# Kernel optimization log

Hardware: AMD Instinct MI355X
Metric: run time of the kernel (lower is better)

The kernel has to match this reference:

```python
import jax, jax.numpy as jnp
import numpy as np

H = 16          # n_heads
EPS = 1e-3      # keras LayerNormalization default epsilon


def _layernorm(x, gamma, beta):
    m = jnp.mean(x, axis=-1, keepdims=True)
    v = jnp.var(x, axis=-1, keepdims=True)
    return (x - m) * jax.lax.rsqrt(v + EPS) * gamma + beta


def _mha(q, k, v, wq, bq, wk, bk, wv, bv, wo, bo, causal):
    B, Sq, D = q.shape
    Sk = k.shape[1]
    d = D // H
    qh = (q @ wq + bq).reshape(B, Sq, H, d)
    kh = (k @ wk + bk).reshape(B, Sk, H, d)
    vh = (v @ wv + bv).reshape(B, Sk, H, d)
    scores = jnp.einsum('bqhd,bkhd->bhqk', qh, kh) / jnp.sqrt(jnp.asarray(d, qh.dtype))
    if causal:
        mask = jnp.tril(jnp.ones((Sq, Sk), dtype=bool))
        scores = jnp.where(mask, scores, jnp.asarray(-1e9, scores.dtype))
    attn = jax.nn.softmax(scores, axis=-1)
    out = jnp.einsum('bhqk,bkhd->bqhd', attn, vh).reshape(B, Sq, D)
    return out @ wo + bo


def setup_inputs() -> dict:
    key = jax.random.key(0)
    B, S, D, DFF = 4, 1024, 1024, 4096
    ks = jax.random.split(key, 16)
    sc = 0.02
    inp = {
        'inputs': jax.random.normal(ks[0], (B, S, D), jnp.float32),
        'enc_outputs': jax.random.normal(ks[1], (B, S, D), jnp.float32),
    }
    # self-attention (mha1)
    inp['wq1'] = jax.random.normal(ks[2], (D, D), jnp.float32) * sc
    inp['wk1'] = jax.random.normal(ks[3], (D, D), jnp.float32) * sc
    inp['wv1'] = jax.random.normal(ks[4], (D, D), jnp.float32) * sc
    inp['wo1'] = jax.random.normal(ks[5], (D, D), jnp.float32) * sc
    inp['bq1'] = jnp.zeros((D,), jnp.float32)
    inp['bk1'] = jnp.zeros((D,), jnp.float32)
    inp['bv1'] = jnp.zeros((D,), jnp.float32)
    inp['bo1'] = jnp.zeros((D,), jnp.float32)
    # cross-attention (mha2)
    inp['wq2'] = jax.random.normal(ks[6], (D, D), jnp.float32) * sc
    inp['wk2'] = jax.random.normal(ks[7], (D, D), jnp.float32) * sc
    inp['wv2'] = jax.random.normal(ks[8], (D, D), jnp.float32) * sc
    inp['wo2'] = jax.random.normal(ks[9], (D, D), jnp.float32) * sc
    inp['bq2'] = jnp.zeros((D,), jnp.float32)
    inp['bk2'] = jnp.zeros((D,), jnp.float32)
    inp['bv2'] = jnp.zeros((D,), jnp.float32)
    inp['bo2'] = jnp.zeros((D,), jnp.float32)
    # FFN
    inp['w_ff1'] = jax.random.normal(ks[10], (D, DFF), jnp.float32) * sc
    inp['b_ff1'] = jnp.zeros((DFF,), jnp.float32)
    inp['w_ff2'] = jax.random.normal(ks[11], (DFF, D), jnp.float32) * sc
    inp['b_ff2'] = jnp.zeros((D,), jnp.float32)
    # LayerNorms
    for i in (1, 2, 3):
        inp[f'g{i}'] = jnp.ones((D,), jnp.float32)
        inp[f'be{i}'] = jnp.zeros((D,), jnp.float32)
    return inp


def reference(inputs, enc_outputs,
              wq1, bq1, wk1, bk1, wv1, bv1, wo1, bo1,
              wq2, bq2, wk2, bk2, wv2, bv2, wo2, bo2,
              w_ff1, b_ff1, w_ff2, b_ff2,
              g1, be1, g2, be2, g3, be3):
    # self-attention block (causal) + residual + LN; dropout is identity (eval)
    a1 = _mha(inputs, inputs, inputs, wq1, bq1, wk1, bk1, wv1, bv1, wo1, bo1, causal=True)
    o1 = _layernorm(inputs + a1, g1, be1)
    # cross-attention block + residual + LN
    a2 = _mha(o1, enc_outputs, enc_outputs, wq2, bq2, wk2, bk2, wv2, bv2, wo2, bo2, causal=False)
    o2 = _layernorm(o1 + a2, g2, be2)
    # FFN block + residual + LN
    f = jax.nn.relu(o2 @ w_ff1 + b_ff1) @ w_ff2 + b_ff2
    return _layernorm(o2 + f, g3, be3)
```

## Files before the change

kernel.cpp:

```cpp
#include <hip/hip_runtime.h>
#include <stdint.h>
#include <stddef.h>

typedef __attribute__((ext_vector_type(4))) float  floatx4;
typedef __attribute__((ext_vector_type(8))) short  short8;
typedef __attribute__((ext_vector_type(4))) short  short4v;

__device__ __forceinline__ float bf2f(short s) {
  union { uint32_t u; float f; } v;
  v.u = ((uint32_t)(uint16_t)s) << 16;
  return v.f;
}
__device__ __forceinline__ short f2bf(float f) {
  union { float f; uint32_t u; } v; v.f = f;
  uint32_t r = v.u + 0x7fffu + ((v.u >> 16) & 1u);
  return (short)(r >> 16);
}

__device__ __forceinline__ void async_cp16(const void* g, void* l) {
  __builtin_amdgcn_global_load_lds(
      (__attribute__((address_space(1))) void*)g,
      (__attribute__((address_space(3))) void*)l, 16, 0, 0);
}

__device__ __forceinline__ int swzb(int row, int bcol) {
  return ((row << 7) + bcol) ^ ((row & 7) << 4);
}

struct TransTable {
  const float* src[10];
  short*       dst[10];
  int K[10], N[10], base[10];
};
__global__ __launch_bounds__(256)
void transpose_all(TransTable tt)
{
  __shared__ short tile[32][33];
  int e = 0;
  #pragma unroll
  for (int i = 1; i < 10; i++) if ((int)blockIdx.x >= tt.base[i]) e = i;
  const int t = blockIdx.x - tt.base[e];
  const int N = tt.N[e], K = tt.K[e];
  const int ncols = N >> 5;
  const int n0 = (t % ncols) << 5, k0 = (t / ncols) << 5;
  const float* src = tt.src[e];
  short* dst = tt.dst[e];
  const int tx = threadIdx.x & 31, ty = threadIdx.x >> 5;
  #pragma unroll
  for (int i = 0; i < 32; i += 8)
    tile[ty + i][tx] = f2bf(src[(size_t)(k0 + ty + i) * N + n0 + tx]);
  __syncthreads();
  #pragma unroll
  for (int i = 0; i < 32; i += 8)
    dst[(size_t)(n0 + ty + i) * K + k0 + tx] = tile[tx][ty + i];
}

__global__ __launch_bounds__(256)
void convert_xe(const float* __restrict__ x, const float* __restrict__ enc,
                short* __restrict__ xc, short* __restrict__ encc)
{
  int b = blockIdx.x;
  const float* s; short* d;
  if (b < 4096) { s = x; d = xc; } else { s = enc; d = encc; b -= 4096; }
  const int i = (b * 256 + threadIdx.x) * 4;
  const floatx4 v = *(const floatx4*)(s + i);
  short4v o;
  #pragma unroll
  for (int j = 0; j < 4; j++) o[j] = f2bf(v[j]);
  *(short4v*)(d + i) = o;
}

struct ParamMap { const float* s[19]; int off[19]; };
__global__ __launch_bounds__(256)
void convert_params(ParamMap pm, short* __restrict__ dst)
{
  const int b = blockIdx.x;
  for (int t = threadIdx.x; t < 1024; t += 256)
    dst[b * 1024 + t] = f2bf(pm.s[b][pm.off[b] + t]);
}

__device__ __forceinline__ void xcd2d(int nbn, int& bm, int& bn) {
  const int x   = (int)blockIdx.x & 7;
  const int loc = (int)blockIdx.x >> 3;
  const int nbm = ((int)gridDim.x) / nbn;
  const int gm  = nbm >> 2;
  const int gn  = nbn >> 1;
  bm = (x >> 1) * gm + loc / gn;
  bn = (x & 1) * gn + loc % gn;
}

template<int RELU, int RESID, int BM, int BN>
__global__ __launch_bounds__(256)
void gemm_bt(const short* __restrict__ A, const short* __restrict__ BT,
             const short* __restrict__ bias, const short* __restrict__ resid,
             short* __restrict__ C, int M, int N, int K)
{
  constexpr int MT = BM / 32;
  constexpr int NT = BN / 32;
  __shared__ short8 As0[BM * 4];
  __shared__ short8 As1[BM * 4];
  __shared__ short8 Bs0[BN * 4];
  __shared__ short8 Bs1[BN * 4];
  const int tid  = threadIdx.x;
  const int w    = tid >> 6;
  const int lane = tid & 63;
  const int m16  = lane & 15;
  const int g    = lane >> 4;
  const int nbn  = N / BN;
  int bm, bn;
  xcd2d(nbn, bm, bn);
  const int wm   = (w >> 1) * (BM / 2);
  const int wn   = (w & 1) * (BN / 2);

  const int r0 = lane >> 2;
  const int c0 = lane & 3;
  const int csw = c0 ^ ((r0 >> 1) & 3);
  const short* pA = A  + (size_t)(bm * BM + w * (BM / 4) + r0) * K + csw * 8;
  const short* pB = BT + (size_t)(bn * BN + w * (BN / 4) + r0) * K + csw * 8;

  floatx4 acc[MT][NT];
  #pragma unroll
  for (int i = 0; i < MT; i++)
    #pragma unroll
    for (int j = 0; j < NT; j++)
      acc[i][j] = floatx4{0.f, 0.f, 0.f, 0.f};

  auto stage = [&](short8* AS, short8* BS, int k0) {
    async_cp16(pA + k0, AS + w * BM);
    if constexpr (BM == 128) async_cp16(pA + k0 + 16 * (size_t)K, AS + w * BM + 64);
    async_cp16(pB + k0, BS + w * BN);
    if constexpr (BN == 128) async_cp16(pB + k0 + 16 * (size_t)K, BS + w * BN + 64);
  };
  const int gs = g ^ ((m16 >> 1) & 3);
  auto compute = [&](const short8* AS, const short8* BS) {
    short8 af[MT], bfr[NT];
    #pragma unroll
    for (int mt = 0; mt < MT; mt++)
      af[mt] = AS[(wm + mt * 16 + m16) * 4 + gs];
    #pragma unroll
    for (int nt = 0; nt < NT; nt++)
      bfr[nt] = BS[(wn + nt * 16 + m16) * 4 + gs];
    #pragma unroll
    for (int mt = 0; mt < MT; mt++)
      #pragma unroll
      for (int nt = 0; nt < NT; nt++)
        acc[mt][nt] = __builtin_amdgcn_mfma_f32_16x16x32_bf16(af[mt], bfr[nt], acc[mt][nt], 0, 0, 0);
  };

  stage(As0, Bs0, 0);
  __syncthreads();

  for (int k0 = 0; k0 < K; k0 += 64) {
    stage(As1, Bs1, k0 + 32);
    compute(As0, Bs0);
    __syncthreads();
    if (k0 + 64 < K)
      stage(As0, Bs0, k0 + 64);
    compute(As1, Bs1);
    __syncthreads();
  }

  #pragma unroll
  for (int mt = 0; mt < MT; mt++) {
    const int rbase = bm * BM + wm + mt * 16 + g * 4;
    #pragma unroll
    for (int nt = 0; nt < NT; nt++) {
      const int col = bn * BN + wn + nt * 16 + m16;
      const float bia = bf2f(bias[col]);
      #pragma unroll
      for (int r = 0; r < 4; r++) {
        const size_t idx = (size_t)(rbase + r) * N + col;
        float v = acc[mt][nt][r] + bia;
        if (RESID) v += bf2f(resid[idx]);
        if (RELU)  v = fmaxf(v, 0.f);
        C[idx] = f2bf(v);
      }
    }
  }
}

template<int RELU, int RESID>
__global__ __launch_bounds__(256)
void gemm_bt64(const short* __restrict__ A, const short* __restrict__ BT,
               const short* __restrict__ bias, const short* __restrict__ resid,
               short* __restrict__ C, int M, int N, int K)
{
  __shared__ short8 As0[512], As1[512];
  __shared__ short8 Bs0[512], Bs1[512];
  const int tid  = threadIdx.x;
  const int w    = tid >> 6;
  const int lane = tid & 63;
  const int m16  = lane & 15;
  const int g    = lane >> 4;
  const int nbn  = N >> 6;
  int bm, bn;
  xcd2d(nbn, bm, bn);
  const int wm   = (w >> 1) << 5;
  const int wn   = (w & 1) << 5;

  const int r0  = lane >> 3;
  const int c0  = lane & 7;
  const int csw = c0 ^ r0;
  const short* pA = A  + (size_t)(bm * 64 + w * 16 + r0) * K + csw * 8;
  const short* pB = BT + (size_t)(bn * 64 + w * 16 + r0) * K + csw * 8;

  floatx4 acc[2][2];
  #pragma unroll
  for (int i = 0; i < 2; i++)
    #pragma unroll
    for (int j = 0; j < 2; j++)
      acc[i][j] = floatx4{0.f, 0.f, 0.f, 0.f};

  auto stage = [&](short8* AS, short8* BS, int k0) {
    async_cp16(pA + k0,                 AS + w * 128);
    async_cp16(pA + k0 + 8 * (size_t)K, AS + w * 128 + 64);
    async_cp16(pB + k0,                 BS + w * 128);
    async_cp16(pB + k0 + 8 * (size_t)K, BS + w * 128 + 64);
  };
  const int sw = m16 & 7;
  auto compute = [&](const short8* AS, const short8* BS) {
    #pragma unroll
    for (int s = 0; s < 2; s++) {
      const int pc = (4 * s + g) ^ sw;
      short8 af[2], bfr[2];
      #pragma unroll
      for (int mt = 0; mt < 2; mt++)
        af[mt] = AS[(wm + mt * 16 + m16) * 8 + pc];
      #pragma unroll
      for (int nt = 0; nt < 2; nt++)
        bfr[nt] = BS[(wn + nt * 16 + m16) * 8 + pc];
      #pragma unroll
      for (int mt = 0; mt < 2; mt++)
        #pragma unroll
        for (int nt = 0; nt < 2; nt++)
          acc[mt][nt] = __builtin_amdgcn_mfma_f32_16x16x32_bf16(af[mt], bfr[nt], acc[mt][nt], 0, 0, 0);
    }
  };

  stage(As0, Bs0, 0);
  __syncthreads();

  for (int k0 = 0; k0 < K; k0 += 128) {
    stage(As1, Bs1, k0 + 64);
    compute(As0, Bs0);
    __syncthreads();
    if (k0 + 128 < K)
      stage(As0, Bs0, k0 + 128);
    compute(As1, Bs1);
    __syncthreads();
  }

  #pragma unroll
  for (int mt = 0; mt < 2; mt++) {
    const int rbase = bm * 64 + wm + mt * 16 + g * 4;
    #pragma unroll
    for (int nt = 0; nt < 2; nt++) {
      const int col = bn * 64 + wn + nt * 16 + m16;
      const float bia = bf2f(bias[col]);
      #pragma unroll
      for (int r = 0; r < 4; r++) {
        const size_t idx = (size_t)(rbase + r) * N + col;
        float v = acc[mt][nt][r] + bia;
        if (RESID) v += bf2f(resid[idx]);
        if (RELU)  v = fmaxf(v, 0.f);
        C[idx] = f2bf(v);
      }
    }
  }
}

template<int CAUSAL>
__global__ __launch_bounds__(256, 4)
void attention(const short* __restrict__ Qp, int ldq,
               const short* __restrict__ Kp, int ldk,
               const short* __restrict__ Vp, int ldv,
               short* __restrict__ Op, int ldo)
{
  const int S   = 1024;
  const int bid = (((int)blockIdx.x & 7) << 7) | ((int)blockIdx.x >> 3);
  const int qt  = bid & 15;
  const int h   = (bid >> 4) & 15;
  const int b   = bid >> 8;
  const int tid = threadIdx.x;
  const int w   = tid >> 6;
  const int lane = tid & 63;
  const int m16 = lane & 15;
  const int g   = lane >> 4;

  __shared__ __align__(16) short Ks[2][64 * 64];
  __shared__ __align__(16) short VT[2][64 * 64];
  __shared__ __align__(16) short Ps[4][16 * 64];

  const int rowQ = b * S + qt * 64;
  const int wrow = w * 16;

  const short* qsrc = Qp + (size_t)(rowQ + wrow + m16) * ldq + h * 64 + 8 * g;
  const short8 qf0 = *(const short8*)qsrc;
  const short8 qf1 = *(const short8*)(qsrc + 32);

  float mrow = -1e38f;
  float lrow = 0.f;
  floatx4 oacc[4];
  #pragma unroll
  for (int dt = 0; dt < 4; dt++) oacc[dt] = floatx4{0.f, 0.f, 0.f, 0.f};

  const int kr  = tid >> 2, kc = (tid & 3) << 4;
  const int vkp = (tid & 31) * 2, vcg = (tid >> 5) << 3;

  const short* kbase = Kp + (size_t)(b * S + kr)  * ldk + h * 64 + kc;
  const short* vbase = Vp + (size_t)(b * S + vkp) * ldv + h * 64 + vcg;

  const int nkt = CAUSAL ? (qt + 1) : (S / 64);
  const int qi  = qt * 64 + wrow + m16;

  short8 kst0 = *(const short8*)kbase;
  short8 kst1 = *(const short8*)(kbase + 8);
  short8 vst0 = *(const short8*)vbase;
  short8 vst1 = *(const short8*)(vbase + ldv);
  {
    char* kd = (char*)&Ks[0][0];
    *(short8*)(kd + swzb(kr, kc * 2))      = kst0;
    *(short8*)(kd + swzb(kr, kc * 2 + 16)) = kst1;
    char* vd = (char*)&VT[0][0];
    #pragma unroll
    for (int j = 0; j < 8; j++) {
      const uint32_t pk = (uint32_t)(uint16_t)vst0[j] | ((uint32_t)(uint16_t)vst1[j] << 16);
      *(uint32_t*)(vd + swzb(vcg + j, vkp * 2)) = pk;
    }
  }
  __syncthreads();

  for (int kt = 0; kt < nkt; kt++) {
    const int cur  = kt & 1;
    const int more = (kt + 1 < nkt);

    if (more) {
      const size_t roff = (size_t)(kt + 1) * 64;
      kst0 = *(const short8*)(kbase + roff * ldk);
      kst1 = *(const short8*)(kbase + roff * ldk + 8);
      vst0 = *(const short8*)(vbase + roff * ldv);
      vst1 = *(const short8*)(vbase + roff * ldv + ldv);
    }

    const int kb = kt * 64;

    const char* ksrc = (const char*)&Ks[cur][0];
    floatx4 sc[4];
    #pragma unroll
    for (int cg4 = 0; cg4 < 4; cg4++) {
      const short8 kfa = *(const short8*)(ksrc + swzb(cg4 * 16 + m16, 16 * g));
      const short8 kfb = *(const short8*)(ksrc + swzb(cg4 * 16 + m16, 64 + 16 * g));
      sc[cg4] = __builtin_amdgcn_mfma_f32_16x16x32_bf16(kfa, qf0, floatx4{0.f,0.f,0.f,0.f}, 0, 0, 0);
      sc[cg4] = __builtin_amdgcn_mfma_f32_16x16x32_bf16(kfb, qf1, sc[cg4], 0, 0, 0);
    }

    float v4[4][4];
    #pragma unroll
    for (int cg = 0; cg < 4; cg++)
      #pragma unroll
      for (int r = 0; r < 4; r++) {
        float x = sc[cg][r] * 0.125f;
        if (CAUSAL && kt == qt) {
          const int key = kb + cg * 16 + g * 4 + r;
          if (key > qi) x = -1e9f;
        }
        v4[cg][r] = x;
      }

    float mx = v4[0][0];
    #pragma unroll
    for (int cg = 0; cg < 4; cg++)
      #pragma unroll
      for (int r = 0; r < 4; r++) mx = fmaxf(mx, v4[cg][r]);
    mx = fmaxf(mx, __shfl_xor(mx, 16));
    mx = fmaxf(mx, __shfl_xor(mx, 32));
    const float mn = fmaxf(mrow, mx);
    const float alpha = __expf(mrow - mn);
    mrow = mn;

    float rs = 0.f;
    #pragma unroll
    for (int cg = 0; cg < 4; cg++)
      #pragma unroll
      for (int r = 0; r < 4; r++) { v4[cg][r] = __expf(v4[cg][r] - mn); rs += v4[cg][r]; }
    rs += __shfl_xor(rs, 16);
    rs += __shfl_xor(rs, 32);
    lrow = lrow * alpha + rs;

    #pragma unroll
    for (int r = 0; r < 4; r++) {
      const float aR = __shfl(alpha, (g << 2) | r);
      #pragma unroll
      for (int dt = 0; dt < 4; dt++) oacc[dt][r] *= aR;
    }

    char* pbase = (char*)&Ps[w][0];
    #pragma unroll
    for (int cg = 0; cg < 4; cg++) {
      const uint32_t p0 = (uint32_t)(uint16_t)f2bf(v4[cg][0]) |
                          ((uint32_t)(uint16_t)f2bf(v4[cg][1]) << 16);
      const uint32_t p1 = (uint32_t)(uint16_t)f2bf(v4[cg][2]) |
                          ((uint32_t)(uint16_t)f2bf(v4[cg][3]) << 16);
      *(uint32_t*)(pbase + swzb(m16, (8 * cg + 2 * g) * 4))     = p0;
      *(uint32_t*)(pbase + swzb(m16, (8 * cg + 2 * g + 1) * 4)) = p1;
    }

    asm volatile("s_waitcnt lgkmcnt(0)" ::: "memory");
    __builtin_amdgcn_sched_barrier(0);

    const short8 pf0 = *(const short8*)(pbase + swzb(m16, 16 * g));
    const short8 pf1 = *(const short8*)(pbase + swzb(m16, 64 + 16 * g));
    const char* vsrc = (const char*)&VT[cur][0];
    #pragma unroll
    for (int dt = 0; dt < 4; dt++) {
      const short8 vfa = *(const short8*)(vsrc + swzb(dt * 16 + m16, 16 * g));
      const short8 vfb = *(const short8*)(vsrc + swzb(dt * 16 + m16, 64 + 16 * g));
      oacc[dt] = __builtin_amdgcn_mfma_f32_16x16x32_bf16(pf0, vfa, oacc[dt], 0, 0, 0);
      oacc[dt] = __builtin_amdgcn_mfma_f32_16x16x32_bf16(pf1, vfb, oacc[dt], 0, 0, 0);
    }

    if (more) {
      char* kd = (char*)&Ks[cur ^ 1][0];
      *(short8*)(kd + swzb(kr, kc * 2))      = kst0;
      *(short8*)(kd + swzb(kr, kc * 2 + 16)) = kst1;
      char* vd = (char*)&VT[cur ^ 1][0];
      #pragma unroll
      for (int j = 0; j < 8; j++) {
        const uint32_t pk = (uint32_t)(uint16_t)vst0[j] | ((uint32_t)(uint16_t)vst1[j] << 16);
        *(uint32_t*)(vd + swzb(vcg + j, vkp * 2)) = pk;
      }
      __syncthreads();
    }
  }

  float lR[4];
  #pragma unroll
  for (int r = 0; r < 4; r++) lR[r] = __shfl(lrow, (g << 2) | r);
  #pragma unroll
  for (int dt = 0; dt < 4; dt++)
    #pragma unroll
    for (int r = 0; r < 4; r++) {
      const size_t orow = (size_t)(rowQ + wrow + g * 4 + r);
      Op[orow * ldo + h * 64 + dt * 16 + m16] = f2bf(oacc[dt][r] / lR[r]);
    }
}

template<int FINAL>
__global__ __launch_bounds__(256)
void layernorm_bf16(const short* __restrict__ x, const short* __restrict__ gamma,
                    const short* __restrict__ beta, void* __restrict__ out)
{
  const int D = 1024;
  const int row = blockIdx.x, tid = threadIdx.x;
  const short* xr = x + (size_t)row * D;
  short4v xv = *(const short4v*)(xr + tid * 4);
  float v[4], s = 0.f, ss = 0.f;
  #pragma unroll
  for (int j = 0; j < 4; j++) { v[j] = bf2f(xv[j]); s += v[j]; ss += v[j] * v[j]; }
  #pragma unroll
  for (int off = 32; off; off >>= 1) { s += __shfl_xor(s, off); ss += __shfl_xor(ss, off); }
  __shared__ float red[8];
  const int w = tid >> 6, lane = tid & 63;
  if (lane == 0) { red[w] = s; red[4 + w] = ss; }
  __syncthreads();
  s  = red[0] + red[1] + red[2] + red[3];
  ss = red[4] + red[5] + red[6] + red[7];
  const float mean = s * (1.f / D);
  const float var  = ss * (1.f / D) - mean * mean;
  const float inv  = rsqrtf(var + 1e-3f);
  float o[4];
  #pragma unroll
  for (int j = 0; j < 4; j++)
    o[j] = (v[j] - mean) * inv * bf2f(gamma[tid * 4 + j]) + bf2f(beta[tid * 4 + j]);
  if (FINAL) {
    floatx4 ov;
    #pragma unroll
    for (int j = 0; j < 4; j++) ov[j] = o[j];
    *(floatx4*)((float*)out + (size_t)row * D + tid * 4) = ov;
  } else {
    short4v ov;
    #pragma unroll
    for (int j = 0; j < 4; j++) ov[j] = f2bf(o[j]);
    *(short4v*)((short*)out + (size_t)row * D + tid * 4) = ov;
  }
}

extern "C" void kernel_launch(void* const* d_in, const int* in_sizes, int n_in,
                              void* d_out, int out_size, void* d_ws, size_t ws_size,
                              hipStream_t stream) {
  (void)in_sizes; (void)n_in; (void)out_size; (void)ws_size;
  const int M = 4096;
  const size_t MM = 1024 * 1024;

  short* ws = (short*)d_ws;
  short* wt_qkv1 = ws;
  short* wt_o1   = wt_qkv1 + 3 * MM;
  short* wt_q2   = wt_o1 + MM;
  short* wt_kv2  = wt_q2 + MM;
  short* wt_o2   = wt_kv2 + 2 * MM;
  short* wt_ff1  = wt_o2 + MM;
  short* wt_ff2  = wt_ff1 + 4 * MM;
  short* P       = ws + 16 * MM;
  short* encc    = ws + 16 * MM + 32768;
  short* act0    = encc + 4 * MM;
  short* attn    = act0 + 16 * MM;
  short* t1      = attn + 4 * MM;
  short* t2      = t1 + 4 * MM;
  short* xc      = t2;

  short* bqkv1 = P,        *bo1  = P + 3072, *bkv2 = P + 4096, *bq2 = P + 6144;
  short* bo2   = P + 7168, *bff1 = P + 8192, *bff2 = P + 12288;
  short* g1 = P + 13312, *be1 = P + 14336, *g2 = P + 15360, *be2 = P + 16384;
  short* g3 = P + 17408, *be3 = P + 18432;

  ParamMap pm;
  const int srcidx[19] = {6, 7, 8, 9, 15, 16, 14, 17, 19, 19, 19, 19, 21, 22, 23, 24, 25, 26, 27};
  const int offs[19]   = {0, 0, 0, 0, 0,  0,  0,  0,  0, 1024, 2048, 3072, 0, 0, 0, 0, 0, 0, 0};
  for (int i = 0; i < 19; i++) { pm.s[i] = (const float*)d_in[srcidx[i]]; pm.off[i] = offs[i]; }
  convert_params<<<19, 256, 0, stream>>>(pm, P);

  convert_xe<<<8192, 256, 0, stream>>>((const float*)d_in[0], (const float*)d_in[1], xc, encc);

  TransTable tt;
  const int widx[10] = {2, 3, 4, 5, 10, 11, 12, 13, 18, 20};
  short* wdst[10] = {wt_qkv1, wt_qkv1 + MM, wt_qkv1 + 2 * MM, wt_o1, wt_q2,
                     wt_kv2, wt_kv2 + MM, wt_o2, wt_ff1, wt_ff2};
  const int wK[10] = {1024, 1024, 1024, 1024, 1024, 1024, 1024, 1024, 1024, 4096};
  const int wN[10] = {1024, 1024, 1024, 1024, 1024, 1024, 1024, 1024, 4096, 1024};
  int base = 0;
  for (int i = 0; i < 10; i++) {
    tt.src[i] = (const float*)d_in[widx[i]];
    tt.dst[i] = wdst[i];
    tt.K[i] = wK[i]; tt.N[i] = wN[i]; tt.base[i] = base;
    base += (wN[i] / 32) * (wK[i] / 32);
  }
  transpose_all<<<base, 256, 0, stream>>>(tt);

  short* qkv1 = act0;
  gemm_bt<0, 0, 128, 128><<<dim3((M / 128) * (3072 / 128)), 256, 0, stream>>>(
      xc, wt_qkv1, bqkv1, nullptr, qkv1, M, 3072, 1024);
  attention<1><<<dim3(1024), 256, 0, stream>>>(
      qkv1, 3072, qkv1 + 1024, 3072, qkv1 + 2048, 3072, attn, 1024);
  gemm_bt64<0, 1><<<dim3((M / 64) * (1024 / 64)), 256, 0, stream>>>(
      attn, wt_o1, bo1, xc, t1, M, 1024, 1024);
  layernorm_bf16<0><<<dim3(4096), 256, 0, stream>>>(t1, g1, be1, t1);

  short* kv2 = act0;
  short* q2  = act0 + 8 * MM;
  gemm_bt<0, 0, 64, 128><<<dim3((M / 64) * (2048 / 128)), 256, 0, stream>>>(
      encc, wt_kv2, bkv2, nullptr, kv2, M, 2048, 1024);
  gemm_bt64<0, 0><<<dim3((M / 64) * (1024 / 64)), 256, 0, stream>>>(
      t1, wt_q2, bq2, nullptr, q2, M, 1024, 1024);
  attention<0><<<dim3(1024), 256, 0, stream>>>(
      q2, 1024, kv2, 2048, kv2 + 1024, 2048, attn, 1024);
  gemm_bt64<0, 1><<<dim3((M / 64) * (1024 / 64)), 256, 0, stream>>>(
      attn, wt_o2, bo2, t1, t2, M, 1024, 1024);
  layernorm_bf16<0><<<dim3(4096), 256, 0, stream>>>(t2, g2, be2, t2);

  short* hidden = act0;
  gemm_bt<1, 0, 128, 128><<<dim3((M / 128) * (4096 / 128)), 256, 0, stream>>>(
      t2, wt_ff1, bff1, nullptr, hidden, M, 4096, 1024);
  gemm_bt64<0, 1><<<dim3((M / 64) * (1024 / 64)), 256, 0, stream>>>(
      hidden, wt_ff2, bff2, t2, attn, M, 1024, 4096);
  layernorm_bf16<1><<<dim3(4096), 256, 0, stream>>>(attn, g3, be3, d_out);
}
```

Before: 487.6 us.

## Process 128 query rows per attention block to reuse K/V tiles

Each attention workgroup now handles a 128-row query tile instead of 64. Every wave computes two 16-row query sub-tiles against the same K and V fragments loaded from LDS. This halves the K/V global loads and LDS staging per query row, and the grid shrinks from 1024 to 512 blocks. The cost is more registers per thread (launch bounds lowered to 2 blocks per SM), fewer blocks to fill the GPU, and more causal load imbalance because the causal key-tile count now grows in steps of 2.

```diff
diff --git a/kernel.cpp b/kernel.cpp
--- a/kernel.cpp
+++ b/kernel.cpp
@@ -270,17 +270,17 @@
 }
 
 template<int CAUSAL>
-__global__ __launch_bounds__(256, 4)
+__global__ __launch_bounds__(256, 2)
 void attention(const short* __restrict__ Qp, int ldq,
                const short* __restrict__ Kp, int ldk,
                const short* __restrict__ Vp, int ldv,
                short* __restrict__ Op, int ldo)
 {
   const int S   = 1024;
-  const int bid = (((int)blockIdx.x & 7) << 7) | ((int)blockIdx.x >> 3);
-  const int qt  = bid & 15;
-  const int h   = (bid >> 4) & 15;
-  const int b   = bid >> 8;
+  const int bid = (((int)blockIdx.x & 7) << 6) | ((int)blockIdx.x >> 3);
+  const int qt  = bid & 7;
+  const int h   = (bid >> 3) & 15;
+  const int b   = bid >> 7;
   const int tid = threadIdx.x;
   const int w   = tid >> 6;
   const int lane = tid & 63;
@@ -289,20 +289,23 @@
 
   __shared__ __align__(16) short Ks[2][64 * 64];
   __shared__ __align__(16) short VT[2][64 * 64];
-  __shared__ __align__(16) short Ps[4][16 * 64];
-
-  const int rowQ = b * S + qt * 64;
-  const int wrow = w * 16;
-
-  const short* qsrc = Qp + (size_t)(rowQ + wrow + m16) * ldq + h * 64 + 8 * g;
-  const short8 qf0 = *(const short8*)qsrc;
-  const short8 qf1 = *(const short8*)(qsrc + 32);
-
-  float mrow = -1e38f;
-  float lrow = 0.f;
-  floatx4 oacc[4];
-  #pragma unroll
-  for (int dt = 0; dt < 4; dt++) oacc[dt] = floatx4{0.f, 0.f, 0.f, 0.f};
+  __shared__ __align__(16) short Ps[4][32 * 64];
+
+  const int rowQ = b * S + qt * 128;
+  const int wrow = w * 32;
+
+  const short* qsrcA = Qp + (size_t)(rowQ + wrow + m16) * ldq + h * 64 + 8 * g;
+  const short* qsrcB = qsrcA + (size_t)16 * ldq;
+  const short8 qfa0 = *(const short8*)qsrcA;
+  const short8 qfa1 = *(const short8*)(qsrcA + 32);
+  const short8 qfb0 = *(const short8*)qsrcB;
+  const short8 qfb1 = *(const short8*)(qsrcB + 32);
+
+  float mA = -1e38f, lA = 0.f;
+  float mB = -1e38f, lB = 0.f;
+  floatx4 oA[4], oB[4];
+  #pragma unroll
+  for (int dt = 0; dt < 4; dt++) { oA[dt] = floatx4{0.f,0.f,0.f,0.f}; oB[dt] = floatx4{0.f,0.f,0.f,0.f}; }
 
   const int kr  = tid >> 2, kc = (tid & 3) << 4;
   const int vkp = (tid & 31) * 2, vcg = (tid >> 5) << 3;
@@ -310,8 +313,9 @@
   const short* kbase = Kp + (size_t)(b * S + kr)  * ldk + h * 64 + kc;
   const short* vbase = Vp + (size_t)(b * S + vkp) * ldv + h * 64 + vcg;
 
-  const int nkt = CAUSAL ? (qt + 1) : (S / 64);
-  const int qi  = qt * 64 + wrow + m16;
+  const int nkt = CAUSAL ? (2 * qt + 2) : (S / 64);
+  const int qiA = qt * 128 + wrow + m16;
+  const int qiB = qiA + 16;
 
   short8 kst0 = *(const short8*)kbase;
   short8 kst1 = *(const short8*)(kbase + 8);
@@ -343,80 +347,128 @@
     }
 
     const int kb = kt * 64;
+    const int domask = CAUSAL && (kt >= 2 * qt);
 
     const char* ksrc = (const char*)&Ks[cur][0];
-    floatx4 sc[4];
+    floatx4 scA[4], scB[4];
     #pragma unroll
     for (int cg4 = 0; cg4 < 4; cg4++) {
       const short8 kfa = *(const short8*)(ksrc + swzb(cg4 * 16 + m16, 16 * g));
       const short8 kfb = *(const short8*)(ksrc + swzb(cg4 * 16 + m16, 64 + 16 * g));
-      sc[cg4] = __builtin_amdgcn_mfma_f32_16x16x32_bf16(kfa, qf0, floatx4{0.f,0.f,0.f,0.f}, 0, 0, 0);
-      sc[cg4] = __builtin_amdgcn_mfma_f32_16x16x32_bf16(kfb, qf1, sc[cg4], 0, 0, 0);
-    }
-
-    float v4[4][4];
-    #pragma unroll
-    for (int cg = 0; cg < 4; cg++)
+      scA[cg4] = __builtin_amdgcn_mfma_f32_16x16x32_bf16(kfa, qfa0, floatx4{0.f,0.f,0.f,0.f}, 0, 0, 0);
+      scA[cg4] = __builtin_amdgcn_mfma_f32_16x16x32_bf16(kfb, qfa1, scA[cg4], 0, 0, 0);
+      scB[cg4] = __builtin_amdgcn_mfma_f32_16x16x32_bf16(kfa, qfb0, floatx4{0.f,0.f,0.f,0.f}, 0, 0, 0);
+      scB[cg4] = __builtin_amdgcn_mfma_f32_16x16x32_bf16(kfb, qfb1, scB[cg4], 0, 0, 0);
+    }
+
+    char* pbase = (char*)&Ps[w][0];
+
+    {
+      float v4[4][4];
+      #pragma unroll
+      for (int cg = 0; cg < 4; cg++)
+        #pragma unroll
+        for (int r = 0; r < 4; r++) {
+          float x = scA[cg][r] * 0.125f;
+          if (domask) { const int key = kb + cg * 16 + g * 4 + r; if (key > qiA) x = -1e9f; }
+          v4[cg][r] = x;
+        }
+      float mx = v4[0][0];
+      #pragma unroll
+      for (int cg = 0; cg < 4; cg++)
+        #pragma unroll
+        for (int r = 0; r < 4; r++) mx = fmaxf(mx, v4[cg][r]);
+      mx = fmaxf(mx, __shfl_xor(mx, 16));
+      mx = fmaxf(mx, __shfl_xor(mx, 32));
+      const float mn = fmaxf(mA, mx);
+      const float alpha = __expf(mA - mn);
+      mA = mn;
+      float rs = 0.f;
+      #pragma unroll
+      for (int cg = 0; cg < 4; cg++)
+        #pragma unroll
+        for (int r = 0; r < 4; r++) { v4[cg][r] = __expf(v4[cg][r] - mn); rs += v4[cg][r]; }
+      rs += __shfl_xor(rs, 16);
+      rs += __shfl_xor(rs, 32);
+      lA = lA * alpha + rs;
       #pragma unroll
       for (int r = 0; r < 4; r++) {
-        float x = sc[cg][r] * 0.125f;
-        if (CAUSAL && kt == qt) {
-          const int key = kb + cg * 16 + g * 4 + r;
-          if (key > qi) x = -1e9f;
+        const float aR = __shfl(alpha, (g << 2) | r);
+        #pragma unroll
+        for (int dt = 0; dt < 4; dt++) oA[dt][r] *= aR;
+      }
+      #pragma unroll
+      for (int cg = 0; cg < 4; cg++) {
+        const uint32_t p0 = (uint32_t)(uint16_t)f2bf(v4[cg][0]) |
+                            ((uint32_t)(uint16_t)f2bf(v4[cg][1]) << 16);
+        const uint32_t p1 = (uint32_t)(uint16_t)f2bf(v4[cg][2]) |
+                            ((uint32_t)(uint16_t)f2bf(v4[cg][3]) << 16);
+        *(uint32_t*)(pbase + swzb(m16, (8 * cg + 2 * g) * 4))     = p0;
+        *(uint32_t*)(pbase + swzb(m16, (8 * cg + 2 * g + 1) * 4)) = p1;
+      }
+    }
+
+    {
+      float v4[4][4];
+      #pragma unroll
+      for (int cg = 0; cg < 4; cg++)
+        #pragma unroll
+        for (int r = 0; r < 4; r++) {
+          float x = scB[cg][r] * 0.125f;
+          if (domask) { const int key = kb + cg * 16 + g * 4 + r; if (key > qiB) x = -1e9f; }
+          v4[cg][r] = x;
         }
-        v4[cg][r] = x;
+      float mx = v4[0][0];
+      #pragma unroll
+      for (int cg = 0; cg < 4; cg++)
+        #pragma unroll
+        for (int r = 0; r < 4; r++) mx = fmaxf(mx, v4[cg][r]);
+      mx = fmaxf(mx, __shfl_xor(mx, 16));
+      mx = fmaxf(mx, __shfl_xor(mx, 32));
+      const float mn = fmaxf(mB, mx);
+      const float alpha = __expf(mB - mn);
+      mB = mn;
+      float rs = 0.f;
+      #pragma unroll
+      for (int cg = 0; cg < 4; cg++)
+        #pragma unroll
+        for (int r = 0; r < 4; r++) { v4[cg][r] = __expf(v4[cg][r] - mn); rs += v4[cg][r]; }
+      rs += __shfl_xor(rs, 16);
+      rs += __shfl_xor(rs, 32);
+      lB = lB * alpha + rs;
+      #pragma unroll
+      for (int r = 0; r < 4; r++) {
+        const float aR = __shfl(alpha, (g << 2) | r);
+        #pragma unroll
+        for (int dt = 0; dt < 4; dt++) oB[dt][r] *= aR;
       }
-
-    float mx = v4[0][0];
-    #pragma unroll
-    for (int cg = 0; cg < 4; cg++)
-      #pragma unroll
-      for (int r = 0; r < 4; r++) mx = fmaxf(mx, v4[cg][r]);
-    mx = fmaxf(mx, __shfl_xor(mx, 16));
-    mx = fmaxf(mx, __shfl_xor(mx, 32));
-    const float mn = fmaxf(mrow, mx);
-    const float alpha = __expf(mrow - mn);
-    mrow = mn;
-
-    float rs = 0.f;
-    #pragma unroll
-    for (int cg = 0; cg < 4; cg++)
-      #pragma unroll
-      for (int r = 0; r < 4; r++) { v4[cg][r] = __expf(v4[cg][r] - mn); rs += v4[cg][r]; }
-    rs += __shfl_xor(rs, 16);
-    rs += __shfl_xor(rs, 32);
-    lrow = lrow * alpha + rs;
-
-    #pragma unroll
-    for (int r = 0; r < 4; r++) {
-      const float aR = __shfl(alpha, (g << 2) | r);
-      #pragma unroll
-      for (int dt = 0; dt < 4; dt++) oacc[dt][r] *= aR;
-    }
-
-    char* pbase = (char*)&Ps[w][0];
-    #pragma unroll
-    for (int cg = 0; cg < 4; cg++) {
-      const uint32_t p0 = (uint32_t)(uint16_t)f2bf(v4[cg][0]) |
-                          ((uint32_t)(uint16_t)f2bf(v4[cg][1]) << 16);
-      const uint32_t p1 = (uint32_t)(uint16_t)f2bf(v4[cg][2]) |
-                          ((uint32_t)(uint16_t)f2bf(v4[cg][3]) << 16);
-      *(uint32_t*)(pbase + swzb(m16, (8 * cg + 2 * g) * 4))     = p0;
-      *(uint32_t*)(pbase + swzb(m16, (8 * cg + 2 * g + 1) * 4)) = p1;
+      #pragma unroll
+      for (int cg = 0; cg < 4; cg++) {
+        const uint32_t p0 = (uint32_t)(uint16_t)f2bf(v4[cg][0]) |
+                            ((uint32_t)(uint16_t)f2bf(v4[cg][1]) << 16);
+        const uint32_t p1 = (uint32_t)(uint16_t)f2bf(v4[cg][2]) |
+                            ((uint32_t)(uint16_t)f2bf(v4[cg][3]) << 16);
+        *(uint32_t*)(pbase + swzb(16 + m16, (8 * cg + 2 * g) * 4))     = p0;
+        *(uint32_t*)(pbase + swzb(16 + m16, (8 * cg + 2 * g + 1) * 4)) = p1;
+      }
     }
 
     asm volatile("s_waitcnt lgkmcnt(0)" ::: "memory");
     __builtin_amdgcn_sched_barrier(0);
 
-    const short8 pf0 = *(const short8*)(pbase + swzb(m16, 16 * g));
-    const short8 pf1 = *(const short8*)(pbase + swzb(m16, 64 + 16 * g));
+    const short8 pfa0 = *(const short8*)(pbase + swzb(m16, 16 * g));
+    const short8 pfa1 = *(const short8*)(pbase + swzb(m16, 64 + 16 * g));
+    const short8 pfb0 = *(const short8*)(pbase + swzb(16 + m16, 16 * g));
+    const short8 pfb1 = *(const short8*)(pbase + swzb(16 + m16, 64 + 16 * g));
     const char* vsrc = (const char*)&VT[cur][0];
     #pragma unroll
     for (int dt = 0; dt < 4; dt++) {
       const short8 vfa = *(const short8*)(vsrc + swzb(dt * 16 + m16, 16 * g));
       const short8 vfb = *(const short8*)(vsrc + swzb(dt * 16 + m16, 64 + 16 * g));
-      oacc[dt] = __builtin_amdgcn_mfma_f32_16x16x32_bf16(pf0, vfa, oacc[dt], 0, 0, 0);
-      oacc[dt] = __builtin_amdgcn_mfma_f32_16x16x32_bf16(pf1, vfb, oacc[dt], 0, 0, 0);
+      oA[dt] = __builtin_amdgcn_mfma_f32_16x16x32_bf16(pfa0, vfa, oA[dt], 0, 0, 0);
+      oA[dt] = __builtin_amdgcn_mfma_f32_16x16x32_bf16(pfa1, vfb, oA[dt], 0, 0, 0);
+      oB[dt] = __builtin_amdgcn_mfma_f32_16x16x32_bf16(pfb0, vfa, oB[dt], 0, 0, 0);
+      oB[dt] = __builtin_amdgcn_mfma_f32_16x16x32_bf16(pfb1, vfb, oB[dt], 0, 0, 0);
     }
 
     if (more) {
@@ -433,15 +485,20 @@
     }
   }
 
-  float lR[4];
-  #pragma unroll
-  for (int r = 0; r < 4; r++) lR[r] = __shfl(lrow, (g << 2) | r);
+  float lRA[4], lRB[4];
+  #pragma unroll
+  for (int r = 0; r < 4; r++) {
+    lRA[r] = __shfl(lA, (g << 2) | r);
+    lRB[r] = __shfl(lB, (g << 2) | r);
+  }
   #pragma unroll
   for (int dt = 0; dt < 4; dt++)
     #pragma unroll
     for (int r = 0; r < 4; r++) {
-      const size_t orow = (size_t)(rowQ + wrow + g * 4 + r);
-      Op[orow * ldo + h * 64 + dt * 16 + m16] = f2bf(oacc[dt][r] / lR[r]);
+      const size_t orowA = (size_t)(rowQ + wrow + g * 4 + r);
+      Op[orowA * ldo + h * 64 + dt * 16 + m16] = f2bf(oA[dt][r] / lRA[r]);
+      const size_t orowB = orowA + 16;
+      Op[orowB * ldo + h * 64 + dt * 16 + m16] = f2bf(oB[dt][r] / lRB[r]);
     }
 }
 
@@ -539,7 +596,7 @@
   short* qkv1 = act0;
   gemm_bt<0, 0, 128, 128><<<dim3((M / 128) * (3072 / 128)), 256, 0, stream>>>(
       xc, wt_qkv1, bqkv1, nullptr, qkv1, M, 3072, 1024);
-  attention<1><<<dim3(1024), 256, 0, stream>>>(
+  attention<1><<<dim3(512), 256, 0, stream>>>(
       qkv1, 3072, qkv1 + 1024, 3072, qkv1 + 2048, 3072, attn, 1024);
   gemm_bt64<0, 1><<<dim3((M / 64) * (1024 / 64)), 256, 0, stream>>>(
       attn, wt_o1, bo1, xc, t1, M, 1024, 1024);
@@ -551,7 +608,7 @@
       encc, wt_kv2, bkv2, nullptr, kv2, M, 2048, 1024);
   gemm_bt64<0, 0><<<dim3((M / 64) * (1024 / 64)), 256, 0, stream>>>(
       t1, wt_q2, bq2, nullptr, q2, M, 1024, 1024);
-  attention<0><<<dim3(1024), 256, 0, stream>>>(
+  attention<0><<<dim3(512), 256, 0, stream>>>(
       q2, 1024, kv2, 2048, kv2 + 1024, 2048, attn, 1024);
   gemm_bt64<0, 1><<<dim3((M / 64) * (1024 / 64)), 256, 0, stream>>>(
       attn, wt_o2, bo2, t1, t2, M, 1024, 1024);
```

Result: no change. 495.6 us (+1.6%).
